# Optimization experiments

Measured on AMD Instinct MI355X. Metric: run time of the kernel, lower is better.

The kernel has to match this reference:

```python
import jax, jax.numpy as jnp
import numpy as np

EPS = 1e-8


def _cdist(a, b):
    # Euclidean pairwise distances [N, M] via ||a||^2 + ||b||^2 - 2 a b^T
    a2 = jnp.sum(a * a, axis=-1, keepdims=True)          # [N, 1]
    b2 = jnp.sum(b * b, axis=-1, keepdims=True).T        # [1, M]
    sq = a2 + b2 - 2.0 * (a @ b.T)                       # [N, M]
    return jnp.sqrt(jnp.maximum(sq, 1e-12))


def setup_inputs() -> dict:
    key = jax.random.key(0)
    k1, k2, k3 = jax.random.split(key, 3)
    N, M = 16384, 16384
    # scale to metric-like LiDAR coordinates
    query_points = jax.random.normal(k1, (N, 3), dtype=jnp.float32) * 20.0
    ref_points = jax.random.normal(k2, (M, 3), dtype=jnp.float32) * 20.0
    ref_flow = jax.random.normal(k3, (M, 3), dtype=jnp.float32)
    return {"query_points": query_points, "ref_points": ref_points,
            "ref_flow": ref_flow, "k": 3}


def reference(query_points, ref_points, ref_flow, k):
    # knn_interpolate_flow (pure-torch fallback path), method='knn'
    dist = _cdist(query_points, ref_points)              # [N, M]
    neg_d, knn_idx = jax.lax.top_k(-dist, k)             # smallest k distances
    knn_dist = -neg_d                                    # [N, k]
    weights = 1.0 / (knn_dist + EPS)
    weights = weights / jnp.sum(weights, axis=1, keepdims=True)
    knn_flow = ref_flow[knn_idx]                         # [N, k, 3]
    interpolated_flow = jnp.sum(weights[..., None] * knn_flow, axis=1)  # [N, 3]
    return interpolated_flow
```

## Files before the change

### kernel.cpp

```cpp
#include <hip/hip_runtime.h>
#include <math.h>

#define BLOCK 256
#define QPT   4
#define CHUNK 512
#define S     64
#define DELTA 0.05f

__device__ __forceinline__ float mul_rn(float a, float b) {
#pragma clang fp contract(off)
    return a * b;
}
__device__ __forceinline__ float add_rn(float a, float b) {
#pragma clang fp contract(off)
    return a + b;
}
__device__ __forceinline__ float sumsq3(float x, float y, float z) {
    return add_rn(add_rn(mul_rn(x, x), mul_rn(y, y)), mul_rn(z, z));
}
__device__ __forceinline__ float med3f(float a, float b, float c) {
    return __builtin_amdgcn_fmed3f(a, b, c);
}

__device__ __forceinline__ void val3_push(float& d0, float& d1, float& d2, float v) {
    d2 = med3f(d1, d2, v);
    d1 = med3f(d0, d1, v);
    d0 = fminf(d0, v);
}

__device__ __forceinline__ void lex3_push(float& d0, float& d1, float& d2,
                                          int& i0, int& i1, int& i2,
                                          float sq, int idx) {
    const bool l0 = (sq < d0) || (sq == d0 && idx < i0);
    const bool l1 = (sq < d1) || (sq == d1 && idx < i1);
    const bool l2 = (sq < d2) || (sq == d2 && idx < i2);
    i2 = l1 ? i1 : (l2 ? idx : i2);
    d2 = l1 ? d1 : (l2 ? sq  : d2);
    i1 = l0 ? i0 : (l1 ? idx : i1);
    d1 = l0 ? d0 : (l1 ? sq  : d1);
    i0 = l0 ? idx : i0;
    d0 = l0 ? sq  : d0;
}

__device__ __forceinline__ void stage_chunk(const float* __restrict__ r,
                                            int start, int cnt,
                                            float4* __restrict__ smem,
                                            float4* __restrict__ g4) {
    const int t = threadIdx.x;
    if (t < (cnt >> 2)) {
        const float4* p = (const float4*)(r + (size_t)(start + t * 4) * 3);
        const float4 A = p[0], B = p[1], C = p[2];
        const float4 o0 = make_float4(-2.0f * A.x, -2.0f * A.y, -2.0f * A.z,
                                      sumsq3(A.x, A.y, A.z));
        const float4 o1 = make_float4(-2.0f * A.w, -2.0f * B.x, -2.0f * B.y,
                                      sumsq3(A.w, B.x, B.y));
        const float4 o2 = make_float4(-2.0f * B.z, -2.0f * B.w, -2.0f * C.x,
                                      sumsq3(B.z, B.w, C.x));
        const float4 o3 = make_float4(-2.0f * C.y, -2.0f * C.z, -2.0f * C.w,
                                      sumsq3(C.y, C.z, C.w));
        smem[t * 4 + 0] = o0;
        smem[t * 4 + 1] = o1;
        smem[t * 4 + 2] = o2;
        smem[t * 4 + 3] = o3;
        if (g4) {
            g4[t * 4 + 0] = o0;
            g4[t * 4 + 1] = o1;
            g4[t * 4 + 2] = o2;
            g4[t * 4 + 3] = o3;
        }
    }
}

__global__ __launch_bounds__(BLOCK, 4) void values_kernel(
    const float* __restrict__ q, const float* __restrict__ r,
    float* __restrict__ smin, float4* __restrict__ r4,
    int N, int refsPerSlice)
{
    __shared__ float4 smem[CHUNK];
    const int tid = threadIdx.x;
    const int s   = blockIdx.y;
    const int start = s * refsPerSlice;

    float a0[QPT], a1[QPT], a2[QPT], an[QPT], d0[QPT];
#pragma unroll
    for (int u = 0; u < QPT; ++u) {
        const int qi = (blockIdx.x * QPT + u) * BLOCK + tid;
        a0[u] = q[qi * 3 + 0];
        a1[u] = q[qi * 3 + 1];
        a2[u] = q[qi * 3 + 2];
        an[u] = sumsq3(a0[u], a1[u], a2[u]);
        d0[u] = __builtin_inff();
    }

    for (int coff = 0; coff < refsPerSlice; coff += CHUNK) {
        const int cnt = min(CHUNK, refsPerSlice - coff);
        __syncthreads();
        stage_chunk(r, start + coff, cnt, smem,
                    (blockIdx.x == 0) ? (r4 + start + coff) : nullptr);
        __syncthreads();
#pragma unroll 4
        for (int j = 0; j < cnt; j += 2) {
            const float4 b0 = smem[j];
            const float4 b1 = smem[j + 1];
#pragma unroll
            for (int u = 0; u < QPT; ++u) {
                const float t0 = __builtin_fmaf(a2[u], b0.z,
                                 __builtin_fmaf(a1[u], b0.y,
                                 __builtin_fmaf(a0[u], b0.x, b0.w)));
                const float t1 = __builtin_fmaf(a2[u], b1.z,
                                 __builtin_fmaf(a1[u], b1.y,
                                 __builtin_fmaf(a0[u], b1.x, b1.w)));
                d0[u] = fminf(fminf(t0, t1), d0[u]);
            }
        }
    }

#pragma unroll
    for (int u = 0; u < QPT; ++u) {
        const int qi = (blockIdx.x * QPT + u) * BLOCK + tid;
        smin[(size_t)qi * S + s] = an[u] + d0[u];
    }
}

__global__ __launch_bounds__(BLOCK, 4) void rescan_kernel(
    const float* __restrict__ q, const float4* __restrict__ r4,
    const float* __restrict__ smin, const float* __restrict__ flow,
    float* __restrict__ out, int N, int refsPerSlice)
{
    const int lane = threadIdx.x & 63;
    const int qi   = blockIdx.x * (BLOCK / 64) + (threadIdx.x >> 6);

    const float a0 = q[qi * 3 + 0];
    const float a1 = q[qi * 3 + 1];
    const float a2 = q[qi * 3 + 2];
    const float an = sumsq3(a0, a1, a2);

    const float v = smin[(size_t)qi * S + lane];
    float g0 = v, g1 = __builtin_inff(), g2 = __builtin_inff();
#pragma unroll
    for (int m = 1; m < 64; m <<= 1) {
        const float e0 = __shfl_xor(g0, m);
        const float e1 = __shfl_xor(g1, m);
        const float e2 = __shfl_xor(g2, m);
        val3_push(g0, g1, g2, e0);
        val3_push(g0, g1, g2, e1);
        val3_push(g0, g1, g2, e2);
    }

    unsigned long long mask = __ballot(v <= g2 + DELTA);

    float d0 = __builtin_inff(), d1 = __builtin_inff(), d2 = __builtin_inff();
    int   i0 = 0x7fffffff, i1 = 0x7fffffff, i2 = 0x7fffffff;
    const int K = refsPerSlice >> 6;

    while (mask) {
        const int s = (int)__builtin_ctzll(mask);
        mask &= mask - 1;
        const int base = s * refsPerSlice;
#pragma unroll 4
        for (int k = 0; k < K; ++k) {
            const int idx = base + lane + (k << 6);
            const float4 b = r4[idx];
            const float d = __builtin_fmaf(a2, b.z,
                            __builtin_fmaf(a1, b.y, mul_rn(a0, b.x)));
            const float sq = add_rn(d, add_rn(an, b.w));
            const bool c0 = sq < d0;
            const bool c1 = sq < d1;
            const bool c2 = sq < d2;
            i2 = c1 ? i1 : (c2 ? idx : i2);
            d2 = c1 ? d1 : (c2 ? sq  : d2);
            i1 = c0 ? i0 : (c1 ? idx : i1);
            d1 = c0 ? d0 : (c1 ? sq  : d1);
            i0 = c0 ? idx : i0;
            d0 = c0 ? sq  : d0;
        }
    }

#pragma unroll
    for (int m = 1; m < 64; m <<= 1) {
        const float e0 = __shfl_xor(d0, m);
        const float e1 = __shfl_xor(d1, m);
        const float e2 = __shfl_xor(d2, m);
        const int   j0 = __shfl_xor(i0, m);
        const int   j1 = __shfl_xor(i1, m);
        const int   j2 = __shfl_xor(i2, m);
        lex3_push(d0, d1, d2, i0, i1, i2, e0, j0);
        lex3_push(d0, d1, d2, i0, i1, i2, e1, j1);
        lex3_push(d0, d1, d2, i0, i1, i2, e2, j2);
    }

    if (lane == 0) {
        const float t0 = sqrtf(fmaxf(d0, 1e-12f));
        const float t1 = sqrtf(fmaxf(d1, 1e-12f));
        const float t2 = sqrtf(fmaxf(d2, 1e-12f));
        const float w0r = 1.0f / add_rn(t0, 1e-8f);
        const float w1r = 1.0f / add_rn(t1, 1e-8f);
        const float w2r = 1.0f / add_rn(t2, 1e-8f);
        const float wsum = add_rn(add_rn(w0r, w1r), w2r);
        const float w0 = w0r / wsum;
        const float w1 = w1r / wsum;
        const float w2 = w2r / wsum;

        const float f00 = flow[3 * i0 + 0], f01 = flow[3 * i0 + 1], f02 = flow[3 * i0 + 2];
        const float f10 = flow[3 * i1 + 0], f11 = flow[3 * i1 + 1], f12 = flow[3 * i1 + 2];
        const float f20 = flow[3 * i2 + 0], f21 = flow[3 * i2 + 1], f22 = flow[3 * i2 + 2];

        out[qi * 3 + 0] = add_rn(add_rn(mul_rn(w0, f00), mul_rn(w1, f10)), mul_rn(w2, f20));
        out[qi * 3 + 1] = add_rn(add_rn(mul_rn(w0, f01), mul_rn(w1, f11)), mul_rn(w2, f21));
        out[qi * 3 + 2] = add_rn(add_rn(mul_rn(w0, f02), mul_rn(w1, f12)), mul_rn(w2, f22));
    }
}

extern "C" void kernel_launch(void* const* d_in, const int* in_sizes, int n_in,
                              void* d_out, int out_size, void* d_ws, size_t ws_size,
                              hipStream_t stream) {
    const float* q    = (const float*)d_in[0];
    const float* r    = (const float*)d_in[1];
    const float* flow = (const float*)d_in[2];

    const int N = in_sizes[0] / 3;
    const int M = in_sizes[1] / 3;

    const int refsPerSlice = M / S;
    float*  smin = (float*)d_ws;
    float4* r4   = (float4*)((char*)d_ws + (size_t)N * S * sizeof(float));
    (void)ws_size;

    dim3 grid1(N / (BLOCK * QPT), S);
    values_kernel<<<grid1, BLOCK, 0, stream>>>(q, r, smin, r4, N, refsPerSlice);

    rescan_kernel<<<N / (BLOCK / 64), BLOCK, 0, stream>>>(
        q, r4, smin, flow, (float*)d_out, N, refsPerSlice);
}
```

Measured before the change: 101.7 us.

## Compute per-slice min distances with split-fp16 MFMA instead of scalar FMAs

The first pass, which finds each query's minimum squared distance per reference slice, now runs on 32x32x16 fp16 MFMA instructions. Query and reference coordinates are split into hi/lo fp16 pairs so the products are close to fp32 accuracy, and the column minimum is folded out of the accumulator registers. The rescan tolerance DELTA is raised from 0.05 to 0.5 to absorb the extra approximation error, which lets more slices pass the filter and get rescanned exactly. The block tiling changes to 256 queries per block, and the reference slice is loaded once into LDS without chunking.

Measured after the change: 96.33 us. 5.3% less time.

```diff
diff --git a/kernel.cpp b/kernel.cpp
--- a/kernel.cpp
+++ b/kernel.cpp
@@ -2,10 +2,11 @@
 #include <math.h>
 
 #define BLOCK 256
-#define QPT   4
-#define CHUNK 512
 #define S     64
-#define DELTA 0.05f
+#define DELTA 0.5f
+
+typedef _Float16 half8 __attribute__((ext_vector_type(8)));
+typedef float    f32x16 __attribute__((ext_vector_type(16)));
 
 __device__ __forceinline__ float mul_rn(float a, float b) {
 #pragma clang fp contract(off)
@@ -42,84 +43,95 @@
     d0 = l0 ? sq  : d0;
 }
 
-__device__ __forceinline__ void stage_chunk(const float* __restrict__ r,
-                                            int start, int cnt,
-                                            float4* __restrict__ smem,
-                                            float4* __restrict__ g4) {
-    const int t = threadIdx.x;
-    if (t < (cnt >> 2)) {
-        const float4* p = (const float4*)(r + (size_t)(start + t * 4) * 3);
-        const float4 A = p[0], B = p[1], C = p[2];
-        const float4 o0 = make_float4(-2.0f * A.x, -2.0f * A.y, -2.0f * A.z,
-                                      sumsq3(A.x, A.y, A.z));
-        const float4 o1 = make_float4(-2.0f * A.w, -2.0f * B.x, -2.0f * B.y,
-                                      sumsq3(A.w, B.x, B.y));
-        const float4 o2 = make_float4(-2.0f * B.z, -2.0f * B.w, -2.0f * C.x,
-                                      sumsq3(B.z, B.w, C.x));
-        const float4 o3 = make_float4(-2.0f * C.y, -2.0f * C.z, -2.0f * C.w,
-                                      sumsq3(C.y, C.z, C.w));
-        smem[t * 4 + 0] = o0;
-        smem[t * 4 + 1] = o1;
-        smem[t * 4 + 2] = o2;
-        smem[t * 4 + 3] = o3;
-        if (g4) {
-            g4[t * 4 + 0] = o0;
-            g4[t * 4 + 1] = o1;
-            g4[t * 4 + 2] = o2;
-            g4[t * 4 + 3] = o3;
-        }
-    }
-}
-
-__global__ __launch_bounds__(BLOCK, 4) void values_kernel(
+__device__ __forceinline__ float fold16(const f32x16 c) {
+    const float A = fminf(fminf(c[0],  c[1]),  c[2]);
+    const float B = fminf(fminf(c[3],  c[4]),  c[5]);
+    const float C = fminf(fminf(c[6],  c[7]),  c[8]);
+    const float D = fminf(fminf(c[9],  c[10]), c[11]);
+    const float E = fminf(fminf(c[12], c[13]), c[14]);
+    const float F = fminf(fminf(A, B), C);
+    const float G = fminf(fminf(D, E), c[15]);
+    return fminf(F, G);
+}
+
+__global__ __launch_bounds__(BLOCK) void values_kernel(
     const float* __restrict__ q, const float* __restrict__ r,
     float* __restrict__ smin, float4* __restrict__ r4,
     int N, int refsPerSlice)
 {
-    __shared__ float4 smem[CHUNK];
+    __shared__ half8 afrag[8][64];
     const int tid = threadIdx.x;
     const int s   = blockIdx.y;
     const int start = s * refsPerSlice;
 
-    float a0[QPT], a1[QPT], a2[QPT], an[QPT], d0[QPT];
-#pragma unroll
-    for (int u = 0; u < QPT; ++u) {
-        const int qi = (blockIdx.x * QPT + u) * BLOCK + tid;
-        a0[u] = q[qi * 3 + 0];
-        a1[u] = q[qi * 3 + 1];
-        a2[u] = q[qi * 3 + 2];
-        an[u] = sumsq3(a0[u], a1[u], a2[u]);
-        d0[u] = __builtin_inff();
-    }
-
-    for (int coff = 0; coff < refsPerSlice; coff += CHUNK) {
-        const int cnt = min(CHUNK, refsPerSlice - coff);
-        __syncthreads();
-        stage_chunk(r, start + coff, cnt, smem,
-                    (blockIdx.x == 0) ? (r4 + start + coff) : nullptr);
-        __syncthreads();
+    for (int j = tid; j < refsPerSlice; j += BLOCK) {
+        const float px = r[3 * (start + j) + 0];
+        const float py = r[3 * (start + j) + 1];
+        const float pz = r[3 * (start + j) + 2];
+        const float mx = -2.0f * px, my = -2.0f * py, mz = -2.0f * pz;
+        const float pw = sumsq3(px, py, pz);
+        const _Float16 mhx = (_Float16)mx, mhy = (_Float16)my, mhz = (_Float16)mz;
+        const _Float16 mlx = (_Float16)(mx - (float)mhx);
+        const _Float16 mly = (_Float16)(my - (float)mhy);
+        const _Float16 mlz = (_Float16)(mz - (float)mhz);
+        const _Float16 pwh = (_Float16)pw;
+        const _Float16 pwl = (_Float16)(pw - (float)pwh);
+        half8 lo, hi;
+        lo[0] = mhx; lo[1] = mhy; lo[2] = mhz; lo[3] = mhx;
+        lo[4] = mhy; lo[5] = mhz; lo[6] = mlx; lo[7] = mly;
+        hi[0] = mlz; hi[1] = pwh; hi[2] = pwl; hi[3] = (_Float16)0;
+        hi[4] = (_Float16)0; hi[5] = (_Float16)0; hi[6] = (_Float16)0; hi[7] = (_Float16)0;
+        afrag[j >> 5][(j & 31)]      = lo;
+        afrag[j >> 5][32 + (j & 31)] = hi;
+        if (blockIdx.x == 0)
+            r4[start + j] = make_float4(mx, my, mz, pw);
+    }
+    __syncthreads();
+
+    const int lane = tid & 63, wave = tid >> 6, col = lane & 31;
+    const int q0 = blockIdx.x * 256 + wave * 64 + col;
+    const int q1 = q0 + 32;
+
+    const float a0x = q[q0 * 3 + 0], a0y = q[q0 * 3 + 1], a0z = q[q0 * 3 + 2];
+    const float a1x = q[q1 * 3 + 0], a1y = q[q1 * 3 + 1], a1z = q[q1 * 3 + 2];
+    const float an0 = sumsq3(a0x, a0y, a0z);
+    const float an1 = sumsq3(a1x, a1y, a1z);
+
+    const _Float16 q0hx = (_Float16)a0x, q0hy = (_Float16)a0y, q0hz = (_Float16)a0z;
+    const _Float16 q0lx = (_Float16)(a0x - (float)q0hx);
+    const _Float16 q0ly = (_Float16)(a0y - (float)q0hy);
+    const _Float16 q0lz = (_Float16)(a0z - (float)q0hz);
+    const _Float16 q1hx = (_Float16)a1x, q1hy = (_Float16)a1y, q1hz = (_Float16)a1z;
+    const _Float16 q1lx = (_Float16)(a1x - (float)q1hx);
+    const _Float16 q1ly = (_Float16)(a1y - (float)q1hy);
+    const _Float16 q1lz = (_Float16)(a1z - (float)q1hz);
+    const _Float16 one = (_Float16)1.0f, zer = (_Float16)0.0f;
+
+    half8 b0, b1;
+    if (lane < 32) {
+        b0[0]=q0hx; b0[1]=q0hy; b0[2]=q0hz; b0[3]=q0lx; b0[4]=q0ly; b0[5]=q0lz; b0[6]=q0hx; b0[7]=q0hy;
+        b1[0]=q1hx; b1[1]=q1hy; b1[2]=q1hz; b1[3]=q1lx; b1[4]=q1ly; b1[5]=q1lz; b1[6]=q1hx; b1[7]=q1hy;
+    } else {
+        b0[0]=q0hz; b0[1]=one; b0[2]=one; b0[3]=zer; b0[4]=zer; b0[5]=zer; b0[6]=zer; b0[7]=zer;
+        b1[0]=q1hz; b1[1]=one; b1[2]=one; b1[3]=zer; b1[4]=zer; b1[5]=zer; b1[6]=zer; b1[7]=zer;
+    }
+
+    const f32x16 Z = {0.f,0.f,0.f,0.f,0.f,0.f,0.f,0.f,0.f,0.f,0.f,0.f,0.f,0.f,0.f,0.f};
+    float rm0 = __builtin_inff(), rm1 = __builtin_inff();
+    const int nt = refsPerSlice >> 5;
 #pragma unroll 4
-        for (int j = 0; j < cnt; j += 2) {
-            const float4 b0 = smem[j];
-            const float4 b1 = smem[j + 1];
-#pragma unroll
-            for (int u = 0; u < QPT; ++u) {
-                const float t0 = __builtin_fmaf(a2[u], b0.z,
-                                 __builtin_fmaf(a1[u], b0.y,
-                                 __builtin_fmaf(a0[u], b0.x, b0.w)));
-                const float t1 = __builtin_fmaf(a2[u], b1.z,
-                                 __builtin_fmaf(a1[u], b1.y,
-                                 __builtin_fmaf(a0[u], b1.x, b1.w)));
-                d0[u] = fminf(fminf(t0, t1), d0[u]);
-            }
-        }
-    }
-
-#pragma unroll
-    for (int u = 0; u < QPT; ++u) {
-        const int qi = (blockIdx.x * QPT + u) * BLOCK + tid;
-        smin[(size_t)qi * S + s] = an[u] + d0[u];
-    }
+    for (int t = 0; t < nt; ++t) {
+        const half8 af = afrag[t][lane];
+        const f32x16 c0 = __builtin_amdgcn_mfma_f32_32x32x16_f16(af, b0, Z, 0, 0, 0);
+        const f32x16 c1 = __builtin_amdgcn_mfma_f32_32x32x16_f16(af, b1, Z, 0, 0, 0);
+        rm0 = fminf(rm0, fold16(c0));
+        rm1 = fminf(rm1, fold16(c1));
+    }
+    rm0 = fminf(rm0, __shfl_xor(rm0, 32));
+    rm1 = fminf(rm1, __shfl_xor(rm1, 32));
+
+    if (lane < 32) smin[(size_t)q0 * S + s] = an0 + rm0;
+    else           smin[(size_t)q1 * S + s] = an1 + rm1;
 }
 
 __global__ __launch_bounds__(BLOCK, 4) void rescan_kernel(
@@ -226,7 +238,7 @@
     float4* r4   = (float4*)((char*)d_ws + (size_t)N * S * sizeof(float));
     (void)ws_size;
 
-    dim3 grid1(N / (BLOCK * QPT), S);
+    dim3 grid1(N / 256, S);
     values_kernel<<<grid1, BLOCK, 0, stream>>>(q, r, smin, r4, N, refsPerSlice);
 
     rescan_kernel<<<N / (BLOCK / 64), BLOCK, 0, stream>>>(
```
